# Kernel tuning notes

Hardware: AMD Instinct MI355X
Metric: run time of the kernel (lower is better)

## Reference

```python
import jax, jax.numpy as jnp
import numpy as np

B, S, D = 2, 2048, 1024
H, DK = 16, 64          # n_heads, d_kv; inner_dim = H*DK = D
NUM_BUCKETS = 32        # T5 relative_attention_num_buckets
MAX_DIST = 128          # T5 relative_attention_max_distance
SM_SCALE = 1.0 / np.sqrt(H)  # module uses 1/sqrt(n_heads), not 1/sqrt(d_kv)


def setup_inputs() -> dict:
    key = jax.random.key(0)
    ks = jax.random.split(key, 6)
    w = 0.02  # typical init scale for projection weights
    return {
        "hidden_states": jax.random.normal(ks[0], (B, S, D), jnp.float32),
        "Wq": jax.random.normal(ks[1], (D, H * DK), jnp.float32) * w,
        "Wk": jax.random.normal(ks[2], (D, H * DK), jnp.float32) * w,
        "Wv": jax.random.normal(ks[3], (D, H * DK), jnp.float32) * w,
        "Wo": jax.random.normal(ks[4], (H * DK, D), jnp.float32) * w,
        "rel_bias": jax.random.normal(ks[5], (NUM_BUCKETS, H), jnp.float32) * w,
    }


def _relative_position_buckets(qlen, klen):
    """T5 bidirectional relative-position bucketing -> [qlen, klen] int32."""
    ctx = jnp.arange(qlen, dtype=jnp.int32)[:, None]
    mem = jnp.arange(klen, dtype=jnp.int32)[None, :]
    rp = mem - ctx  # relative position
    nb = NUM_BUCKETS // 2  # bidirectional split
    ret = (rp > 0).astype(jnp.int32) * nb
    rpa = jnp.abs(rp)
    max_exact = nb // 2
    is_small = rpa < max_exact
    rpf = jnp.maximum(rpa, 1).astype(jnp.float32)
    large = max_exact + (
        jnp.log(rpf / max_exact) / np.log(MAX_DIST / max_exact) * (nb - max_exact)
    ).astype(jnp.int32)
    large = jnp.minimum(large, nb - 1)
    return ret + jnp.where(is_small, rpa, large)


def reference(hidden_states, Wq, Wk, Wv, Wo, rel_bias):
    b, s, d = hidden_states.shape
    q = (hidden_states @ Wq).reshape(b, s, H, DK)
    k = (hidden_states @ Wk).reshape(b, s, H, DK)
    v = (hidden_states @ Wv).reshape(b, s, H, DK)

    buckets = _relative_position_buckets(s, s)        # [S, S]
    bias = rel_bias[buckets]                          # [S, S, H]
    bias = jnp.transpose(bias, (2, 0, 1))[None]       # [1, H, S, S]

    scores = jnp.einsum("bqhd,bkhd->bhqk", q, k) * SM_SCALE + bias
    attn = jax.nn.softmax(scores, axis=-1)
    out = jnp.einsum("bhqk,bkhd->bqhd", attn, v).reshape(b, s, H * DK)
    return out @ Wo
```

## Files before the change

kernel.cpp:

```cpp
#include <hip/hip_runtime.h>
#include <math.h>


typedef _Float16 f16;
typedef _Float16 f16x4 __attribute__((ext_vector_type(4)));
typedef _Float16 f16x8 __attribute__((ext_vector_type(8)));
typedef float f32x4 __attribute__((ext_vector_type(4)));

#define MFMA16(a, b, c) __builtin_amdgcn_mfma_f32_16x16x32_f16((a), (b), (c), 0, 0, 0)

static __device__ __forceinline__ float EXP2(float x) {
  float r;
  asm("v_exp_f32 %0, %1" : "=v"(r) : "v"(x));
  return r;
}

__device__ __forceinline__ void gload16(const f16* g, f16* l) {
  __builtin_amdgcn_global_load_lds(
      (const __attribute__((address_space(1))) void*)g,
      (__attribute__((address_space(3))) void*)l, 16, 0, 0);
}


__global__ __launch_bounds__(256) void cast_x_kernel(const float4* __restrict__ x,
                                                     f16x4* __restrict__ xh) {
  int i = blockIdx.x * 256 + threadIdx.x;
  float4 v = x[i];
  f16x4 o;
  o[0] = (f16)v.x; o[1] = (f16)v.y; o[2] = (f16)v.z; o[3] = (f16)v.w;
  xh[i] = o;
}

__global__ void transpose_w_kernel(const float* __restrict__ w0, const float* __restrict__ w1,
                                   const float* __restrict__ w2, const float* __restrict__ w3,
                                   f16* __restrict__ wt) {
  int z = blockIdx.z;
  const float* w = (z == 0) ? w0 : (z == 1) ? w1 : (z == 2) ? w2 : w3;
  float sc = (z == 0) ? 0.36067376022224085f : 1.0f;
  __shared__ float tile[32][33];
  int tx = threadIdx.x, ty = threadIdx.y;
  int kt = blockIdx.x * 32, nt = blockIdx.y * 32;
#pragma unroll
  for (int i = 0; i < 4; ++i)
    tile[ty + i * 8][tx] = w[(size_t)(kt + ty + i * 8) * 1024 + nt + tx];
  __syncthreads();
#pragma unroll
  for (int i = 0; i < 4; ++i)
    wt[((size_t)z * 1024 + nt + ty + i * 8) * 1024 + kt + tx] = (f16)(tile[tx][ty + i * 8] * sc);
}

__global__ __launch_bounds__(256) void bias_kernel(const float* __restrict__ rel_bias,
                                                   f16* __restrict__ bias_rel) {
  int idx = blockIdx.x * 256 + threadIdx.x;
  int h = idx >> 12;
  int r = idx & 4095;
  int rp = r - 2048;
  if (rp < -2047) rp = -2047;
  int bucket = (rp > 0) ? 16 : 0;
  int rpa = (rp < 0) ? -rp : rp;
  if (rpa < 8) {
    bucket += rpa;
  } else {
    int large = 8 + (int)(logf((float)rpa / 8.0f) / logf(16.0f) * 8.0f);
    bucket += (large < 15) ? large : 15;
  }
  bias_rel[idx] = (f16)(rel_bias[bucket * 16 + h] * 1.4426950408889634f);
}

__device__ __forceinline__ void gemm128_core(const f16* __restrict__ A, const f16* __restrict__ Bt,
                                             int mrow, int ncol0, f16* sm ,
                                             f32x4 acc[4][4]) {
  const int t = threadIdx.x;
  const int lane = t & 63, w = t >> 6;
  const int cL = lane & 15, g = lane >> 4;
  const int wr = w >> 1, wc = w & 1;

  const int c0 = w * 128 + lane;
  const int c1 = c0 + 64;
  const int rA0 = c0 >> 2, kA0 = ((c0 & 3) ^ (rA0 & 3)) << 3;
  const int rA1 = c1 >> 2, kA1 = ((c1 & 3) ^ (rA1 & 3)) << 3;
  const f16* gA0 = A + (size_t)(mrow + rA0) * 1024 + kA0;
  const f16* gA1 = A + (size_t)(mrow + rA1) * 1024 + kA1;
  const f16* gB0 = Bt + (size_t)(ncol0 + rA0) * 1024 + kA0;
  const f16* gB1 = Bt + (size_t)(ncol0 + rA1) * 1024 + kA1;
  const int lds0 = (w * 2) * 512, lds1 = (w * 2 + 1) * 512;

#define GSTAGE(buf, k0)                            \
  do {                                             \
    f16* s_ = sm + (buf) * 8192;                   \
    gload16(gA0 + (k0), s_ + lds0);                \
    gload16(gA1 + (k0), s_ + lds1);                \
    gload16(gB0 + (k0), s_ + 4096 + lds0);         \
    gload16(gB1 + (k0), s_ + 4096 + lds1);         \
  } while (0)

  GSTAGE(0, 0);
  __syncthreads();
#pragma unroll 2
  for (int ks = 0; ks < 32; ++ks) {
    const int cur = ks & 1;
    if (ks < 31) GSTAGE(cur ^ 1, (ks + 1) * 32);
    const f16* bA = sm + cur * 8192;
    const f16* bB = bA + 4096;
    f16x8 af[4], bf[4];
#pragma unroll
    for (int m = 0; m < 4; ++m) {
      int r = wr * 64 + m * 16 + cL;
      af[m] = *(const f16x8*)&bA[r * 32 + ((g ^ (r & 3)) << 3)];
    }
#pragma unroll
    for (int n = 0; n < 4; ++n) {
      int r = wc * 64 + n * 16 + cL;
      bf[n] = *(const f16x8*)&bB[r * 32 + ((g ^ (r & 3)) << 3)];
    }
#pragma unroll
    for (int m = 0; m < 4; ++m)
#pragma unroll
      for (int n = 0; n < 4; ++n) acc[m][n] = MFMA16(af[m], bf[n], acc[m][n]);
    __syncthreads();
  }
#undef GSTAGE
}

__global__ __launch_bounds__(256) void gemm_qkv_kernel(const f16* __restrict__ Xh,
                                                       const f16* __restrict__ Wt,
                                                       f16* __restrict__ Qh,
                                                       f16* __restrict__ Kh,
                                                       f16* __restrict__ Vt) {
  __shared__ __align__(16) f16 sm[2][8192];
  int mrow = blockIdx.y * 128, ncol0 = blockIdx.x * 128;
  f32x4 acc[4][4] = {};
  gemm128_core(Xh, Wt, mrow, ncol0, &sm[0][0], acc);
  int lane = threadIdx.x & 63, w = threadIdx.x >> 6;
  int cL = lane & 15, g = lane >> 4;
  int wr = w >> 1, wc = w & 1;
  int which = (ncol0 + wc * 64) >> 10;
#pragma unroll
  for (int m = 0; m < 4; ++m) {
#pragma unroll
    for (int n = 0; n < 4; ++n) {
#pragma unroll
      for (int r = 0; r < 4; ++r) {
        int tt = mrow + wr * 64 + m * 16 + g * 4 + r;
        int b = tt >> 11, s = tt & 2047;
        int col = (ncol0 + wc * 64 + n * 16 + cL) & 1023;
        int hh = col >> 6, dk = col & 63;
        f16 val = (f16)acc[m][n][r];
        if (which == 0)
          Qh[(((size_t)b * 16 + hh) * 2048 + s) * 64 + dk] = val;
        else if (which == 1)
          Kh[(((size_t)b * 16 + hh) * 2048 + s) * 64 + dk] = val;
        else
          Vt[(((size_t)b * 16 + hh) * 64 + dk) * 2048 + s] = val;
      }
    }
  }
}

__global__ __launch_bounds__(256) void gemm_out_kernel(const f16* __restrict__ Oh,
                                                       const f16* __restrict__ WoT,
                                                       float* __restrict__ out) {
  __shared__ __align__(16) f16 sm[2][8192];
  int mrow = blockIdx.y * 128, ncol0 = blockIdx.x * 128;
  f32x4 acc[4][4] = {};
  gemm128_core(Oh, WoT, mrow, ncol0, &sm[0][0], acc);
  int lane = threadIdx.x & 63, w = threadIdx.x >> 6;
  int cL = lane & 15, g = lane >> 4;
  int wr = w >> 1, wc = w & 1;
#pragma unroll
  for (int m = 0; m < 4; ++m)
#pragma unroll
    for (int n = 0; n < 4; ++n)
#pragma unroll
      for (int r = 0; r < 4; ++r) {
        int tt = mrow + wr * 64 + m * 16 + g * 4 + r;
        out[(size_t)tt * 1024 + ncol0 + wc * 64 + n * 16 + cL] = acc[m][n][r];
      }
}

__global__ __launch_bounds__(256) void attn_kernel(const f16* __restrict__ Qh,
                                                   const f16* __restrict__ Kh,
                                                   const f16* __restrict__ Vt,
                                                   const f16* __restrict__ bias_rel,
                                                   f16* __restrict__ Oh) {
  __shared__ __align__(16) f16 sKV[2][8192];
  __shared__ __align__(16) char sP[4][4096];
  __shared__ __align__(16) f16 sB[2176];
  int bh = blockIdx.y;
  int h = bh & 15, b = bh >> 4;
  int qt = blockIdx.x * 128;
  int t = threadIdx.x;
  int lane = t & 63, wave = t >> 6;
  int cL = lane & 15, g = lane >> 4;
  const size_t bhS = (size_t)bh * 2048;
  const int qbase = qt + wave * 32;

  const f16* qp = Qh + (bhS + qbase + cL) * 64 + 8 * g;
  f16x8 qa00 = *(const f16x8*)qp;
  f16x8 qa01 = *(const f16x8*)(qp + 32);
  f16x8 qa10 = *(const f16x8*)(qp + 1024);
  f16x8 qa11 = *(const f16x8*)(qp + 1056);

  float cpos = (float)bias_rel[(size_t)h * 4096 + 4095];
  float cneg = (float)bias_rel[(size_t)h * 4096 + 1];

  {
    const float4* gB = (const float4*)(bias_rel + (size_t)h * 4096 + 1920 - qt);
    for (int i = t; i < 272; i += 256) ((float4*)sB)[i] = gB[i];
  }

  const int rK0 = t >> 3, ccK0 = ((t & 7) ^ (rK0 & 7)) << 3;
  const int rK1 = rK0 + 32, ccK1 = ((t & 7) ^ (rK1 & 7)) << 3;
  const f16* gK0 = Kh + (bhS + rK0) * 64 + ccK0;
  const f16* gK1 = Kh + (bhS + rK1) * 64 + ccK1;
  const f16* gV0 = Vt + ((size_t)bh * 64 + rK0) * 2048 + ccK0;
  const f16* gV1 = Vt + ((size_t)bh * 64 + rK1) * 2048 + ccK1;
  const int ldsA = wave * 512, ldsB = wave * 512 + 2048;

#define ASTAGE(buf, key0)                           \
  do {                                              \
    f16* s_ = &sKV[buf][0];                         \
    gload16(gK0 + (size_t)(key0) * 64, s_ + ldsA);  \
    gload16(gK1 + (size_t)(key0) * 64, s_ + ldsB);  \
    gload16(gV0 + (key0), s_ + 4096 + ldsA);        \
    gload16(gV1 + (key0), s_ + 4096 + ldsB);        \
  } while (0)

  f32x4 o0[4] = {}, o1[4] = {};
  float m0 = -INFINITY, m1 = -INFINITY, lsum0 = 0.f, lsum1 = 0.f;
  char* pbase = sP[wave];
  const int sw = (cL & 7) << 4;
  const int pw0 = cL * 128;

  ASTAGE(0, 0);
  __syncthreads();
  for (int kt = 0; kt < 32; ++kt) {
    const int cur = kt & 1;
    if (kt < 31) ASTAGE(cur ^ 1, (kt + 1) * 64);
    const int key0 = kt * 64;
    const f16* kb = &sKV[cur][0];
    const f16* vb = kb + 4096;
    const int dkt = key0 - qt;

    f16x8 kf0[4], kf1[4];
#pragma unroll
    for (int n = 0; n < 4; ++n) {
      int key = n * 16 + cL;
      kf0[n] = *(const f16x8*)&kb[key * 64 + ((g ^ (key & 7)) << 3)];
      kf1[n] = *(const f16x8*)&kb[key * 64 + (((g + 4) ^ (key & 7)) << 3)];
    }
    f32x4 sa0[4], sa1[4];
    if (dkt >= 256 || dkt <= -192) {
      float c = (dkt > 0) ? cpos : cneg;
#pragma unroll
      for (int n = 0; n < 4; ++n)
#pragma unroll
        for (int r = 0; r < 4; ++r) { sa0[n][r] = c; sa1[n][r] = c; }
    } else {
      const int bb0 = key0 + g * 4 + 128 - wave * 32 - cL;
      const int bb1 = bb0 - 16;
#pragma unroll
      for (int n = 0; n < 4; ++n)
#pragma unroll
        for (int r = 0; r < 4; ++r) {
          sa0[n][r] = (float)sB[bb0 + n * 16 + r];
          sa1[n][r] = (float)sB[bb1 + n * 16 + r];
        }
    }
    __builtin_amdgcn_s_setprio(1);
#pragma unroll
    for (int n = 0; n < 4; ++n) {
      sa0[n] = MFMA16(kf0[n], qa00, sa0[n]);
      sa0[n] = MFMA16(kf1[n], qa01, sa0[n]);
      sa1[n] = MFMA16(kf0[n], qa10, sa1[n]);
      sa1[n] = MFMA16(kf1[n], qa11, sa1[n]);
    }
    __builtin_amdgcn_s_setprio(0);
    float mx0 = fmaxf(fmaxf(fmaxf(sa0[0][0], sa0[0][1]), fmaxf(sa0[0][2], sa0[0][3])),
                      fmaxf(fmaxf(sa0[1][0], sa0[1][1]), fmaxf(sa0[1][2], sa0[1][3])));
    mx0 = fmaxf(mx0, fmaxf(fmaxf(fmaxf(sa0[2][0], sa0[2][1]), fmaxf(sa0[2][2], sa0[2][3])),
                           fmaxf(fmaxf(sa0[3][0], sa0[3][1]), fmaxf(sa0[3][2], sa0[3][3]))));
    float mx1 = fmaxf(fmaxf(fmaxf(sa1[0][0], sa1[0][1]), fmaxf(sa1[0][2], sa1[0][3])),
                      fmaxf(fmaxf(sa1[1][0], sa1[1][1]), fmaxf(sa1[1][2], sa1[1][3])));
    mx1 = fmaxf(mx1, fmaxf(fmaxf(fmaxf(sa1[2][0], sa1[2][1]), fmaxf(sa1[2][2], sa1[2][3])),
                           fmaxf(fmaxf(sa1[3][0], sa1[3][1]), fmaxf(sa1[3][2], sa1[3][3]))));
    mx0 = fmaxf(mx0, __shfl_xor(mx0, 16));
    mx0 = fmaxf(mx0, __shfl_xor(mx0, 32));
    mx1 = fmaxf(mx1, __shfl_xor(mx1, 16));
    mx1 = fmaxf(mx1, __shfl_xor(mx1, 32));
    if (__any((mx0 > m0 + 8.f) || (mx1 > m1 + 8.f))) {
      float mn0 = fmaxf(m0, mx0), mn1 = fmaxf(m1, mx1);
      float corr0 = EXP2(m0 - mn0), corr1 = EXP2(m1 - mn1);
      lsum0 *= corr0; lsum1 *= corr1;
      m0 = mn0; m1 = mn1;
#pragma unroll
      for (int r = 0; r < 4; ++r) {
        float c0 = __shfl(corr0, g * 4 + r);
        float c1 = __shfl(corr1, g * 4 + r);
#pragma unroll
        for (int n = 0; n < 4; ++n) { o0[n][r] *= c0; o1[n][r] *= c1; }
      }
    }
#pragma unroll
    for (int n = 0; n < 4; ++n) {
      f16x4 pk0, pk1;
#pragma unroll
      for (int r = 0; r < 4; ++r) {
        float p0 = EXP2(sa0[n][r] - m0);
        float p1 = EXP2(sa1[n][r] - m1);
        lsum0 += p0; lsum1 += p1;
        pk0[r] = (f16)p0; pk1[r] = (f16)p1;
      }
      *(f16x4*)(pbase + pw0 + ((n * 32 + g * 8) ^ sw)) = pk0;
      *(f16x4*)(pbase + 2048 + pw0 + ((n * 32 + g * 8) ^ sw)) = pk1;
    }
    asm volatile("s_waitcnt lgkmcnt(0)" ::: "memory");
    f16x8 pa00 = *(const f16x8*)(pbase + pw0 + ((g * 16) ^ sw));
    f16x8 pa01 = *(const f16x8*)(pbase + pw0 + ((64 + g * 16) ^ sw));
    f16x8 pa10 = *(const f16x8*)(pbase + 2048 + pw0 + ((g * 16) ^ sw));
    f16x8 pa11 = *(const f16x8*)(pbase + 2048 + pw0 + ((64 + g * 16) ^ sw));
    __builtin_amdgcn_s_setprio(1);
#pragma unroll
    for (int n = 0; n < 4; ++n) {
      int dk = n * 16 + cL;
      f16x8 v0 = *(const f16x8*)&vb[dk * 64 + ((g ^ (dk & 7)) << 3)];
      f16x8 v1 = *(const f16x8*)&vb[dk * 64 + (((g + 4) ^ (dk & 7)) << 3)];
      o0[n] = MFMA16(pa00, v0, o0[n]);
      o0[n] = MFMA16(pa01, v1, o0[n]);
      o1[n] = MFMA16(pa10, v0, o1[n]);
      o1[n] = MFMA16(pa11, v1, o1[n]);
    }
    __builtin_amdgcn_s_setprio(0);
    __syncthreads();
  }
#undef ASTAGE
  lsum0 += __shfl_xor(lsum0, 16);
  lsum0 += __shfl_xor(lsum0, 32);
  lsum1 += __shfl_xor(lsum1, 16);
  lsum1 += __shfl_xor(lsum1, 32);
  float inv0 = 1.0f / lsum0, inv1 = 1.0f / lsum1;
  const int qrow0 = qbase + g * 4;
  size_t rowoff = ((size_t)b * 2048 + qrow0) * 1024 + h * 64;
#pragma unroll
  for (int r = 0; r < 4; ++r) {
    float iv0 = __shfl(inv0, g * 4 + r);
    float iv1 = __shfl(inv1, g * 4 + r);
#pragma unroll
    for (int n = 0; n < 4; ++n) {
      Oh[rowoff + (size_t)r * 1024 + n * 16 + cL] = (f16)(o0[n][r] * iv0);
      Oh[rowoff + (size_t)(r + 16) * 1024 + n * 16 + cL] = (f16)(o1[n][r] * iv1);
    }
  }
}


extern "C" void kernel_launch(void* const* d_in, const int* in_sizes, int n_in,
                              void* d_out, int out_size, void* d_ws, size_t ws_size,
                              hipStream_t stream) {
  const float* X = (const float*)d_in[0];
  const float* Wq = (const float*)d_in[1];
  const float* Wk = (const float*)d_in[2];
  const float* Wv = (const float*)d_in[3];
  const float* Wo = (const float*)d_in[4];
  const float* relb = (const float*)d_in[5];

  const size_t MB8 = (size_t)8 << 20;
  if (ws_size < 6 * MB8 + (1 << 19)) return;

  char* ws = (char*)d_ws;
  f16* Xh = (f16*)(ws + 0 * MB8);
  f16* Wt = (f16*)(ws + 1 * MB8);
  f16* Qh = (f16*)(ws + 2 * MB8);
  f16* Kh = (f16*)(ws + 3 * MB8);
  f16* Vt = (f16*)(ws + 4 * MB8);
  f16* Oh = (f16*)(ws + 5 * MB8);
  f16* brel = (f16*)(ws + 6 * MB8);

  cast_x_kernel<<<dim3(4096), dim3(256), 0, stream>>>((const float4*)X, (f16x4*)Xh);
  transpose_w_kernel<<<dim3(32, 32, 4), dim3(32, 8), 0, stream>>>(Wq, Wk, Wv, Wo, Wt);
  bias_kernel<<<dim3(256), dim3(256), 0, stream>>>(relb, brel);
  gemm_qkv_kernel<<<dim3(24, 32), dim3(256), 0, stream>>>(Xh, Wt, Qh, Kh, Vt);
  attn_kernel<<<dim3(16, 32), dim3(256), 0, stream>>>(Qh, Kh, Vt, brel, Oh);
  gemm_out_kernel<<<dim3(8, 32), dim3(256), 0, stream>>>(Oh, Wt + (size_t)3072 * 1024,
                                                         (float*)d_out);
}
```

Baseline: 154.8 us.

## Switch attention to 32x32x16 MFMA with in-register P via permlane32 swap

```diff
diff --git a/kernel.cpp b/kernel.cpp
--- a/kernel.cpp
+++ b/kernel.cpp
@@ -6,13 +6,24 @@
 typedef _Float16 f16x4 __attribute__((ext_vector_type(4)));
 typedef _Float16 f16x8 __attribute__((ext_vector_type(8)));
 typedef float f32x4 __attribute__((ext_vector_type(4)));
+typedef float f32x16 __attribute__((ext_vector_type(16)));
+typedef unsigned int u32;
+typedef u32 u32x4 __attribute__((ext_vector_type(4)));
 
 #define MFMA16(a, b, c) __builtin_amdgcn_mfma_f32_16x16x32_f16((a), (b), (c), 0, 0, 0)
+#define MFMA32(a, b, c) __builtin_amdgcn_mfma_f32_32x32x16_f16((a), (b), (c), 0, 0, 0)
 
 static __device__ __forceinline__ float EXP2(float x) {
   float r;
   asm("v_exp_f32 %0, %1" : "=v"(r) : "v"(x));
   return r;
+}
+
+static __device__ __forceinline__ u32 pk2(float a, float b) {
+  return __builtin_bit_cast(u32, __builtin_amdgcn_cvt_pkrtz(a, b));
+}
+static __device__ __forceinline__ void swap32(u32& a, u32& b) {
+  asm volatile("v_permlane32_swap_b32 %0, %1" : "+v"(a), "+v"(b));
 }
 
 __device__ __forceinline__ void gload16(const f16* g, f16* l) {
@@ -184,22 +195,20 @@
                                                    const f16* __restrict__ bias_rel,
                                                    f16* __restrict__ Oh) {
   __shared__ __align__(16) f16 sKV[2][8192];
-  __shared__ __align__(16) char sP[4][4096];
   __shared__ __align__(16) f16 sB[2176];
   int bh = blockIdx.y;
   int h = bh & 15, b = bh >> 4;
   int qt = blockIdx.x * 128;
   int t = threadIdx.x;
   int lane = t & 63, wave = t >> 6;
-  int cL = lane & 15, g = lane >> 4;
+  int lo5 = lane & 31, hi = lane >> 5;
   const size_t bhS = (size_t)bh * 2048;
-  const int qbase = qt + wave * 32;
-
-  const f16* qp = Qh + (bhS + qbase + cL) * 64 + 8 * g;
-  f16x8 qa00 = *(const f16x8*)qp;
-  f16x8 qa01 = *(const f16x8*)(qp + 32);
-  f16x8 qa10 = *(const f16x8*)(qp + 1024);
-  f16x8 qa11 = *(const f16x8*)(qp + 1056);
+  const int qrow = qt + wave * 32 + lo5;
+
+  const f16* qp = Qh + (bhS + qrow) * 64 + hi * 8;
+  f16x8 qf[4];
+#pragma unroll
+  for (int m = 0; m < 4; ++m) qf[m] = *(const f16x8*)(qp + 16 * m);
 
   float cpos = (float)bias_rel[(size_t)h * 4096 + 4095];
   float cneg = (float)bias_rel[(size_t)h * 4096 + 1];
@@ -226,11 +235,9 @@
     gload16(gV1 + (key0), s_ + 4096 + ldsB);        \
   } while (0)
 
-  f32x4 o0[4] = {}, o1[4] = {};
-  float m0 = -INFINITY, m1 = -INFINITY, lsum0 = 0.f, lsum1 = 0.f;
-  char* pbase = sP[wave];
-  const int sw = (cL & 7) << 4;
-  const int pw0 = cL * 128;
+  f32x16 o0 = {}, o1 = {};
+  float m_ = -INFINITY, lsum = 0.f;
+  const int sw7 = lo5 & 7;
 
   ASTAGE(0, 0);
   __syncthreads();
@@ -242,114 +249,119 @@
     const f16* vb = kb + 4096;
     const int dkt = key0 - qt;
 
-    f16x8 kf0[4], kf1[4];
-#pragma unroll
-    for (int n = 0; n < 4; ++n) {
-      int key = n * 16 + cL;
-      kf0[n] = *(const f16x8*)&kb[key * 64 + ((g ^ (key & 7)) << 3)];
-      kf1[n] = *(const f16x8*)&kb[key * 64 + (((g + 4) ^ (key & 7)) << 3)];
-    }
-    f32x4 sa0[4], sa1[4];
+    f32x16 sa0, sa1;
     if (dkt >= 256 || dkt <= -192) {
       float c = (dkt > 0) ? cpos : cneg;
 #pragma unroll
-      for (int n = 0; n < 4; ++n)
-#pragma unroll
-        for (int r = 0; r < 4; ++r) { sa0[n][r] = c; sa1[n][r] = c; }
+      for (int i = 0; i < 16; ++i) { sa0[i] = c; sa1[i] = c; }
     } else {
-      const int bb0 = key0 + g * 4 + 128 - wave * 32 - cL;
-      const int bb1 = bb0 - 16;
-#pragma unroll
-      for (int n = 0; n < 4; ++n)
-#pragma unroll
-        for (int r = 0; r < 4; ++r) {
-          sa0[n][r] = (float)sB[bb0 + n * 16 + r];
-          sa1[n][r] = (float)sB[bb1 + n * 16 + r];
-        }
-    }
+      const int bb = key0 + 4 * hi - wave * 32 - lo5 + 128;
+#pragma unroll
+      for (int i = 0; i < 16; ++i) {
+        int pat = (i & 3) + 8 * (i >> 2);
+        sa0[i] = (float)sB[bb + pat];
+        sa1[i] = (float)sB[bb + 32 + pat];
+      }
+    }
+    const f16* kr0 = kb + lo5 * 64;
+    const f16* kr1 = kb + (32 + lo5) * 64;
     __builtin_amdgcn_s_setprio(1);
 #pragma unroll
-    for (int n = 0; n < 4; ++n) {
-      sa0[n] = MFMA16(kf0[n], qa00, sa0[n]);
-      sa0[n] = MFMA16(kf1[n], qa01, sa0[n]);
-      sa1[n] = MFMA16(kf0[n], qa10, sa1[n]);
-      sa1[n] = MFMA16(kf1[n], qa11, sa1[n]);
+    for (int m = 0; m < 4; ++m) {
+      int c = ((2 * m + hi) ^ sw7) << 3;
+      sa0 = MFMA32(*(const f16x8*)(kr0 + c), qf[m], sa0);
+      sa1 = MFMA32(*(const f16x8*)(kr1 + c), qf[m], sa1);
     }
     __builtin_amdgcn_s_setprio(0);
-    float mx0 = fmaxf(fmaxf(fmaxf(sa0[0][0], sa0[0][1]), fmaxf(sa0[0][2], sa0[0][3])),
-                      fmaxf(fmaxf(sa0[1][0], sa0[1][1]), fmaxf(sa0[1][2], sa0[1][3])));
-    mx0 = fmaxf(mx0, fmaxf(fmaxf(fmaxf(sa0[2][0], sa0[2][1]), fmaxf(sa0[2][2], sa0[2][3])),
-                           fmaxf(fmaxf(sa0[3][0], sa0[3][1]), fmaxf(sa0[3][2], sa0[3][3]))));
-    float mx1 = fmaxf(fmaxf(fmaxf(sa1[0][0], sa1[0][1]), fmaxf(sa1[0][2], sa1[0][3])),
-                      fmaxf(fmaxf(sa1[1][0], sa1[1][1]), fmaxf(sa1[1][2], sa1[1][3])));
-    mx1 = fmaxf(mx1, fmaxf(fmaxf(fmaxf(sa1[2][0], sa1[2][1]), fmaxf(sa1[2][2], sa1[2][3])),
-                           fmaxf(fmaxf(sa1[3][0], sa1[3][1]), fmaxf(sa1[3][2], sa1[3][3]))));
-    mx0 = fmaxf(mx0, __shfl_xor(mx0, 16));
-    mx0 = fmaxf(mx0, __shfl_xor(mx0, 32));
-    mx1 = fmaxf(mx1, __shfl_xor(mx1, 16));
-    mx1 = fmaxf(mx1, __shfl_xor(mx1, 32));
-    if (__any((mx0 > m0 + 8.f) || (mx1 > m1 + 8.f))) {
-      float mn0 = fmaxf(m0, mx0), mn1 = fmaxf(m1, mx1);
-      float corr0 = EXP2(m0 - mn0), corr1 = EXP2(m1 - mn1);
-      lsum0 *= corr0; lsum1 *= corr1;
-      m0 = mn0; m1 = mn1;
-#pragma unroll
-      for (int r = 0; r < 4; ++r) {
-        float c0 = __shfl(corr0, g * 4 + r);
-        float c1 = __shfl(corr1, g * 4 + r);
-#pragma unroll
-        for (int n = 0; n < 4; ++n) { o0[n][r] *= c0; o1[n][r] *= c1; }
-      }
-    }
-#pragma unroll
-    for (int n = 0; n < 4; ++n) {
-      f16x4 pk0, pk1;
-#pragma unroll
-      for (int r = 0; r < 4; ++r) {
-        float p0 = EXP2(sa0[n][r] - m0);
-        float p1 = EXP2(sa1[n][r] - m1);
-        lsum0 += p0; lsum1 += p1;
-        pk0[r] = (f16)p0; pk1[r] = (f16)p1;
-      }
-      *(f16x4*)(pbase + pw0 + ((n * 32 + g * 8) ^ sw)) = pk0;
-      *(f16x4*)(pbase + 2048 + pw0 + ((n * 32 + g * 8) ^ sw)) = pk1;
-    }
-    asm volatile("s_waitcnt lgkmcnt(0)" ::: "memory");
-    f16x8 pa00 = *(const f16x8*)(pbase + pw0 + ((g * 16) ^ sw));
-    f16x8 pa01 = *(const f16x8*)(pbase + pw0 + ((64 + g * 16) ^ sw));
-    f16x8 pa10 = *(const f16x8*)(pbase + 2048 + pw0 + ((g * 16) ^ sw));
-    f16x8 pa11 = *(const f16x8*)(pbase + 2048 + pw0 + ((64 + g * 16) ^ sw));
+    float tm[16];
+#pragma unroll
+    for (int i = 0; i < 16; ++i) tm[i] = fmaxf(sa0[i], sa1[i]);
+#pragma unroll
+    for (int s2 = 8; s2; s2 >>= 1)
+#pragma unroll
+      for (int i = 0; i < 8; ++i)
+        if (i < s2) tm[i] = fmaxf(tm[i], tm[i + s2]);
+    float mx = fmaxf(tm[0], __shfl_xor(tm[0], 32));
+    if (__any(mx > m_ + 8.f)) {
+      float mn = fmaxf(m_, mx);
+      float corr = EXP2(m_ - mn);
+      lsum *= corr;
+      m_ = mn;
+#pragma unroll
+      for (int i = 0; i < 16; ++i) { o0[i] *= corr; o1[i] *= corr; }
+    }
+    float p[16];
+    u32 w0, w1, w2, w3, w4, w5, w6, w7;
+#pragma unroll
+    for (int i = 0; i < 16; ++i) p[i] = EXP2(sa0[i] - m_);
+    w0 = pk2(p[0], p[1]);   w1 = pk2(p[2], p[3]);
+    w2 = pk2(p[4], p[5]);   w3 = pk2(p[6], p[7]);
+    w4 = pk2(p[8], p[9]);   w5 = pk2(p[10], p[11]);
+    w6 = pk2(p[12], p[13]); w7 = pk2(p[14], p[15]);
+#pragma unroll
+    for (int s2 = 8; s2; s2 >>= 1)
+#pragma unroll
+      for (int i = 0; i < 8; ++i)
+        if (i < s2) p[i] += p[i + s2];
+    float ls = p[0];
+    swap32(w0, w2); swap32(w1, w3); swap32(w4, w6); swap32(w5, w7);
+    f16x8 pb0 = __builtin_bit_cast(f16x8, (u32x4){w0, w1, w2, w3});
+    f16x8 pb1 = __builtin_bit_cast(f16x8, (u32x4){w4, w5, w6, w7});
+#pragma unroll
+    for (int i = 0; i < 16; ++i) p[i] = EXP2(sa1[i] - m_);
+    w0 = pk2(p[0], p[1]);   w1 = pk2(p[2], p[3]);
+    w2 = pk2(p[4], p[5]);   w3 = pk2(p[6], p[7]);
+    w4 = pk2(p[8], p[9]);   w5 = pk2(p[10], p[11]);
+    w6 = pk2(p[12], p[13]); w7 = pk2(p[14], p[15]);
+#pragma unroll
+    for (int s2 = 8; s2; s2 >>= 1)
+#pragma unroll
+      for (int i = 0; i < 8; ++i)
+        if (i < s2) p[i] += p[i + s2];
+    lsum += ls + p[0];
+    swap32(w0, w2); swap32(w1, w3); swap32(w4, w6); swap32(w5, w7);
+    f16x8 pb2 = __builtin_bit_cast(f16x8, (u32x4){w0, w1, w2, w3});
+    f16x8 pb3 = __builtin_bit_cast(f16x8, (u32x4){w4, w5, w6, w7});
+    const f16* vr0 = vb + lo5 * 64;
+    const f16* vr1 = vb + (32 + lo5) * 64;
     __builtin_amdgcn_s_setprio(1);
-#pragma unroll
-    for (int n = 0; n < 4; ++n) {
-      int dk = n * 16 + cL;
-      f16x8 v0 = *(const f16x8*)&vb[dk * 64 + ((g ^ (dk & 7)) << 3)];
-      f16x8 v1 = *(const f16x8*)&vb[dk * 64 + (((g + 4) ^ (dk & 7)) << 3)];
-      o0[n] = MFMA16(pa00, v0, o0[n]);
-      o0[n] = MFMA16(pa01, v1, o0[n]);
-      o1[n] = MFMA16(pa10, v0, o1[n]);
-      o1[n] = MFMA16(pa11, v1, o1[n]);
+    {
+      int c = ((0 + hi) ^ sw7) << 3;
+      o0 = MFMA32(*(const f16x8*)(vr0 + c), pb0, o0);
+      o1 = MFMA32(*(const f16x8*)(vr1 + c), pb0, o1);
+    }
+    {
+      int c = ((2 + hi) ^ sw7) << 3;
+      o0 = MFMA32(*(const f16x8*)(vr0 + c), pb1, o0);
+      o1 = MFMA32(*(const f16x8*)(vr1 + c), pb1, o1);
+    }
+    {
+      int c = ((4 + hi) ^ sw7) << 3;
+      o0 = MFMA32(*(const f16x8*)(vr0 + c), pb2, o0);
+      o1 = MFMA32(*(const f16x8*)(vr1 + c), pb2, o1);
+    }
+    {
+      int c = ((6 + hi) ^ sw7) << 3;
+      o0 = MFMA32(*(const f16x8*)(vr0 + c), pb3, o0);
+      o1 = MFMA32(*(const f16x8*)(vr1 + c), pb3, o1);
     }
     __builtin_amdgcn_s_setprio(0);
     __syncthreads();
   }
 #undef ASTAGE
-  lsum0 += __shfl_xor(lsum0, 16);
-  lsum0 += __shfl_xor(lsum0, 32);
-  lsum1 += __shfl_xor(lsum1, 16);
-  lsum1 += __shfl_xor(lsum1, 32);
-  float inv0 = 1.0f / lsum0, inv1 = 1.0f / lsum1;
-  const int qrow0 = qbase + g * 4;
-  size_t rowoff = ((size_t)b * 2048 + qrow0) * 1024 + h * 64;
-#pragma unroll
-  for (int r = 0; r < 4; ++r) {
-    float iv0 = __shfl(inv0, g * 4 + r);
-    float iv1 = __shfl(inv1, g * 4 + r);
-#pragma unroll
-    for (int n = 0; n < 4; ++n) {
-      Oh[rowoff + (size_t)r * 1024 + n * 16 + cL] = (f16)(o0[n][r] * iv0);
-      Oh[rowoff + (size_t)(r + 16) * 1024 + n * 16 + cL] = (f16)(o1[n][r] * iv1);
-    }
+  lsum += __shfl_xor(lsum, 32);
+  float inv = 1.0f / lsum;
+  size_t base = ((size_t)b * 2048 + qrow) * 1024 + h * 64 + 4 * hi;
+#pragma unroll
+  for (int rq = 0; rq < 4; ++rq) {
+    f16x4 v0, v1;
+#pragma unroll
+    for (int j = 0; j < 4; ++j) {
+      v0[j] = (f16)(o0[rq * 4 + j] * inv);
+      v1[j] = (f16)(o1[rq * 4 + j] * inv);
+    }
+    *(f16x4*)&Oh[base + 8 * rq] = v0;
+    *(f16x4*)&Oh[base + 32 + 8 * rq] = v1;
   }
 }
 
```

Result: faster. 150.1 us (-3.1%).
